# Kernel optimization log

Measured on AMD Instinct MI355X. Metric: run time of the kernel, lower is better.

## Reference

```python
import jax, jax.numpy as jnp
import numpy as np

ANGSTROM2BOHR = 1.8897261258369282
CUTOFF_ANGSTROM = 5.2  # module's `cutoff` init arg, converted to bohr in forward


def smooth_cutoff(d, rc):
    # torchani 'smooth' cutoff: exp(1 - 1/(1 - (d/rc)^2)) for d < rc, else 0
    x2 = (d / rc) ** 2
    x2_safe = jnp.where(x2 < 1.0, x2, 0.0)  # avoid inf inside the masked branch
    return jnp.where(d < rc, jnp.exp(1.0 - 1.0 / (1.0 - x2_safe)), 0.0)


def setup_inputs() -> dict:
    key = jax.random.key(0)
    k0, k1, k2, k3 = jax.random.split(key, 4)
    n_mol, n_atoms, n_pairs = 4096, 64, 16 * 1024 * 1024
    n_elem = 4  # H, C, N, O
    species = jax.random.randint(k0, (n_mol, n_atoms), 0, n_elem)
    energies = jnp.zeros((n_mol,), jnp.float32)
    atom_index12 = jax.random.randint(k1, (2, n_pairs), 0, n_mol * n_atoms)
    distances = jax.random.uniform(k2, (n_pairs,), jnp.float32, 0.5, 6.0)  # angstrom
    # exp_prefactor = -scaling_charge * sqrt(outer(Z, Z)) / 2, Z = [1, 6, 7, 8]
    z = jnp.array([1.0, 6.0, 7.0, 8.0], jnp.float32)
    exp_prefactor = (-0.016 * jnp.sqrt(jnp.outer(z, z)) / 2.0).astype(jnp.float32)
    # distances_factor = -scaling_radius / cutoff_radii (symmetric pairwise radii table)
    radii = jax.random.uniform(k3, (n_elem, n_elem), jnp.float32, 2.0, 5.0)
    radii = 0.5 * (radii + radii.T)
    distances_factor = (-10.0 / radii).astype(jnp.float32)
    return {
        "species": species,
        "energies": energies,
        "atom_index12": atom_index12,
        "distances": distances,
        "exp_prefactor": exp_prefactor,
        "distances_factor": distances_factor,
    }


def reference(species, energies, atom_index12, distances, exp_prefactor, distances_factor):
    n_mol, n_atoms = species.shape
    d = distances * ANGSTROM2BOHR  # [P]
    species12 = species.reshape(-1)[atom_index12]  # [2, P] gather
    pre = exp_prefactor[species12[0], species12[1]]   # [P]
    dfac = distances_factor[species12[0], species12[1]]  # [P]
    srb = pre * jnp.exp(dfac * d)
    srb = srb * smooth_cutoff(d, CUTOFF_ANGSTROM * ANGSTROM2BOHR)
    mol_idx = atom_index12[0] // n_atoms  # [P]
    out = energies + jax.ops.segment_sum(srb, mol_idx, num_segments=n_mol)
    return species, out
```

## Files before the change

kernel.cpp:

```cpp
#include <hip/hip_runtime.h>
#include <math.h>


#define NT        1024
#define NBLK      512
#define SCALE_F   134217728.0f
#define INV_SCALE 7.450580596923828125e-9

typedef unsigned v4u __attribute__((ext_vector_type(4)));
typedef float    v4f __attribute__((ext_vector_type(4)));

__global__ void pack_species_kernel(const int* __restrict__ sp,
                                    unsigned* __restrict__ packed, int nwords) {
    int w = blockIdx.x * blockDim.x + threadIdx.x;
    if (w >= nwords) return;
    const int4* p4 = (const int4*)(sp + (w << 4));
    int4 a = p4[0], b = p4[1], c = p4[2], d = p4[3];
    unsigned v =
        (unsigned)(a.x & 3)        | ((unsigned)(a.y & 3) << 2)  |
        ((unsigned)(a.z & 3) << 4) | ((unsigned)(a.w & 3) << 6)  |
        ((unsigned)(b.x & 3) << 8) | ((unsigned)(b.y & 3) << 10) |
        ((unsigned)(b.z & 3) << 12)| ((unsigned)(b.w & 3) << 14) |
        ((unsigned)(c.x & 3) << 16)| ((unsigned)(c.y & 3) << 18) |
        ((unsigned)(c.z & 3) << 20)| ((unsigned)(c.w & 3) << 22) |
        ((unsigned)(d.x & 3) << 24)| ((unsigned)(d.y & 3) << 26) |
        ((unsigned)(d.z & 3) << 28)| ((unsigned)(d.w & 3) << 30);
    packed[w] = v;
}

__global__ void init_kernel(const int* __restrict__ species,
                            float* __restrict__ out,
                            unsigned long long* __restrict__ acc,
                            int n_species, int n_mol) {
    int i = blockIdx.x * blockDim.x + threadIdx.x;
    if (i < n_species) out[i] = (float)species[i];
    if (i < n_mol)     acc[i] = 0ull;
}

#define GLOAD(d0, d1, dd, OFF)                                              \
    asm volatile("global_load_dwordx4 %0, %3, %4\n\t"                        \
                 "global_load_dwordx4 %1, %3, %5\n\t"                        \
                 "global_load_dwordx4 %2, %3, %6"                            \
                 : "=&v"(d0), "=&v"(d1), "=&v"(dd)                           \
                 : "v"(OFF), "s"(pb0), "s"(pb1), "s"(pbd)                    \
                 : "memory")

#define VWAIT(n)                                                             \
    do {                                                                     \
        asm volatile("s_waitcnt vmcnt(" #n ")" ::: "memory");                \
        __builtin_amdgcn_sched_barrier(0);                                   \
    } while (0)

__global__ __launch_bounds__(NT, 8)
void srb_fused_u32_pipe(const unsigned* __restrict__ packed_ws,
                        const int* __restrict__ ai,
                        const float* __restrict__ dist,
                        const float* __restrict__ pre_tab,
                        const float* __restrict__ dfac_tab,
                        unsigned long long* __restrict__ acc,
                        int P, int mol_shift, int nit) {
    __shared__ unsigned packed[16384];
    __shared__ unsigned binsu[4096];

    const int t = threadIdx.x;
    for (int i = t; i < 4096; i += NT) binsu[i] = 0u;

    const float myPre  = -pre_tab[t & 15];
    const float myDfac =  dfac_tab[t & 15];

    {
        int4* dst = (int4*)packed;
        const int4* src = (const int4*)packed_ws;
        for (int i = t; i < 4096; i += NT) dst[i] = src[i];
    }
    __syncthreads();

    const float a2b   = (float)1.8897261258369282;
    const float rc    = (float)(5.2 * 1.8897261258369282);
    const float rcinv = (float)(1.0 / (5.2 * 1.8897261258369282));

    const int      stride = (int)gridDim.x * NT;
    const unsigned stepB  = (unsigned)stride * 16u;
    unsigned off = (unsigned)((int)blockIdx.x * NT + t) * 16u;

    const char* pb0 = (const char*)ai;
    const char* pb1 = (const char*)(ai + P);
    const char* pbd = (const char*)dist;

    #define PBODY(X0, X1, XD)                                                \
    do {                                                                     \
        unsigned a0_[4] = { X0[0], X0[1], X0[2], X0[3] };                    \
        unsigned a1_[4] = { X1[0], X1[1], X1[2], X1[3] };                    \
        float    dd_[4] = { XD[0], XD[1], XD[2], XD[3] };                    \
        unsigned w0_[4], w1_[4];                                             \
        _Pragma("unroll")                                                    \
        for (int k = 0; k < 4; ++k) w0_[k] = packed[a0_[k] >> 4];            \
        _Pragma("unroll")                                                    \
        for (int k = 0; k < 4; ++k) w1_[k] = packed[a1_[k] >> 4];            \
        float pr_[4], df_[4];                                                \
        _Pragma("unroll")                                                    \
        for (int k = 0; k < 4; ++k) {                                        \
            unsigned s0 = (w0_[k] >> ((a0_[k] & 15u) << 1)) & 3u;            \
            unsigned s1 = (w1_[k] >> ((a1_[k] & 15u) << 1)) & 3u;            \
            int idx = (int)((s0 << 2) | s1);                                 \
            pr_[k] = __shfl(myPre,  idx, 64);                                \
            df_[k] = __shfl(myDfac, idx, 64);                                \
        }                                                                    \
        unsigned q_[4];                                                      \
        _Pragma("unroll")                                                    \
        for (int k = 0; k < 4; ++k) {                                        \
            float db  = dd_[k] * a2b;                                        \
            float x   = db * rcinv;                                          \
            float arg = df_[k] * db + (1.0f - 1.0f / (1.0f - x * x));        \
            float mag = pr_[k] * __expf(arg);                                \
            mag = (db < rc) ? mag : 0.0f;                                    \
            q_[k] = (unsigned)(mag * SCALE_F);                               \
        }                                                                    \
        _Pragma("unroll")                                                    \
        for (int k = 0; k < 4; ++k)                                          \
            atomicAdd(&binsu[a0_[k] >> mol_shift], q_[k]);                   \
    } while (0)

    v4u A0, A1, B0, B1, C0, C1;
    v4f AD, BDv, CD;

    GLOAD(A0, A1, AD, off);  off += stepB;
    GLOAD(B0, B1, BDv, off); off += stepB;

    int i = 0;
    #pragma unroll 1
    for (; i + 4 < nit; i += 3) {
        GLOAD(C0, C1, CD, off);  off += stepB;
        VWAIT(6);
        PBODY(A0, A1, AD);
        GLOAD(A0, A1, AD, off);  off += stepB;
        VWAIT(6);
        PBODY(B0, B1, BDv);
        GLOAD(B0, B1, BDv, off); off += stepB;
        VWAIT(6);
        PBODY(C0, C1, CD);
    }
    VWAIT(3);
    PBODY(A0, A1, AD);
    VWAIT(0);
    PBODY(B0, B1, BDv);

    #undef PBODY

    __syncthreads();
    for (int i2 = t; i2 < 4096; i2 += NT) {
        unsigned v = binsu[i2];
        if (v) atomicAdd(&acc[i2], (unsigned long long)v);
    }
}

__global__ __launch_bounds__(NT, 8)
void srb_fused_u32_gen(const unsigned* __restrict__ packed_ws,
                       const int* __restrict__ ai,
                       const float* __restrict__ dist,
                       const float* __restrict__ pre_tab,
                       const float* __restrict__ dfac_tab,
                       unsigned long long* __restrict__ acc,
                       int P, int mol_shift) {
    __shared__ unsigned packed[16384];
    __shared__ unsigned binsu[4096];

    const int t = threadIdx.x;
    for (int i = t; i < 4096; i += NT) binsu[i] = 0u;
    const float myPre  = -pre_tab[t & 15];
    const float myDfac =  dfac_tab[t & 15];
    {
        int4* dst = (int4*)packed;
        const int4* src = (const int4*)packed_ws;
        for (int i = t; i < 4096; i += NT) dst[i] = src[i];
    }
    __syncthreads();

    const float a2b   = (float)1.8897261258369282;
    const float rc    = (float)(5.2 * 1.8897261258369282);
    const float rcinv = (float)(1.0 / (5.2 * 1.8897261258369282));

    const int ng     = P >> 2;
    const int stride = (int)gridDim.x * NT;
    const int4*   v0 = (const int4*)ai;
    const int4*   v1 = (const int4*)(ai + P);
    const float4* dv = (const float4*)dist;

    for (int g = (int)blockIdx.x * NT + t; g < ng; g += stride) {
        int4 I0 = v0[g], I1 = v1[g]; float4 D = dv[g];
        unsigned a0[4] = { (unsigned)I0.x, (unsigned)I0.y,
                           (unsigned)I0.z, (unsigned)I0.w };
        unsigned a1[4] = { (unsigned)I1.x, (unsigned)I1.y,
                           (unsigned)I1.z, (unsigned)I1.w };
        float    dd[4] = { D.x, D.y, D.z, D.w };
        unsigned w0[4], w1[4];
        #pragma unroll
        for (int k = 0; k < 4; ++k) w0[k] = packed[a0[k] >> 4];
        #pragma unroll
        for (int k = 0; k < 4; ++k) w1[k] = packed[a1[k] >> 4];
        float pr[4], df[4];
        #pragma unroll
        for (int k = 0; k < 4; ++k) {
            unsigned s0 = (w0[k] >> ((a0[k] & 15u) << 1)) & 3u;
            unsigned s1 = (w1[k] >> ((a1[k] & 15u) << 1)) & 3u;
            int idx = (int)((s0 << 2) | s1);
            pr[k] = __shfl(myPre,  idx, 64);
            df[k] = __shfl(myDfac, idx, 64);
        }
        unsigned q[4];
        #pragma unroll
        for (int k = 0; k < 4; ++k) {
            float db  = dd[k] * a2b;
            float x   = db * rcinv;
            float arg = df[k] * db + (1.0f - 1.0f / (1.0f - x * x));
            float mag = pr[k] * __expf(arg);
            mag = (db < rc) ? mag : 0.0f;
            q[k] = (unsigned)(mag * SCALE_F);
        }
        #pragma unroll
        for (int k = 0; k < 4; ++k)
            atomicAdd(&binsu[a0[k] >> mol_shift], q[k]);
    }

    __syncthreads();
    for (int i = t; i < 4096; i += NT) {
        unsigned v = binsu[i];
        if (v) atomicAdd(&acc[i], (unsigned long long)v);
    }
}

__global__ void final_kernel(const unsigned long long* __restrict__ acc,
                             const float* __restrict__ energies,
                             float* __restrict__ out_e, int n_mol) {
    int m = blockIdx.x * blockDim.x + threadIdx.x;
    if (m < n_mol)
        out_e[m] = energies[m] - (float)((double)acc[m] * INV_SCALE);
}

__global__ void init_out_fallback(const int* __restrict__ species,
                                  const float* __restrict__ energies,
                                  float* __restrict__ out,
                                  int n_species, int n_mol) {
    int i = blockIdx.x * blockDim.x + threadIdx.x;
    if (i < n_species) out[i] = (float)species[i];
    else if (i < n_species + n_mol) out[i] = energies[i - n_species];
}

__global__ __launch_bounds__(NT, 1)
void srb_fused_f32(const int* __restrict__ species,
                   const int* __restrict__ ai,
                   const float* __restrict__ dist,
                   const float* __restrict__ pre_tab,
                   const float* __restrict__ dfac_tab,
                   float* __restrict__ out_e,
                   int P, int mol_shift) {
    __shared__ unsigned packed[16384];
    __shared__ float bins[4096];
    __shared__ float2 tab[16];
    const int t = threadIdx.x;
    for (int i = t; i < 4096; i += NT) bins[i] = 0.0f;
    if (t < 16) tab[t] = make_float2(pre_tab[t], dfac_tab[t]);
    for (int w = t; w < 16384; w += NT) {
        const int4* p4 = (const int4*)(species + (w << 4));
        int4 a = p4[0], b = p4[1], c = p4[2], d = p4[3];
        unsigned v =
            (unsigned)(a.x & 3)        | ((unsigned)(a.y & 3) << 2)  |
            ((unsigned)(a.z & 3) << 4) | ((unsigned)(a.w & 3) << 6)  |
            ((unsigned)(b.x & 3) << 8) | ((unsigned)(b.y & 3) << 10) |
            ((unsigned)(b.z & 3) << 12)| ((unsigned)(b.w & 3) << 14) |
            ((unsigned)(c.x & 3) << 16)| ((unsigned)(c.y & 3) << 18) |
            ((unsigned)(c.z & 3) << 20)| ((unsigned)(c.w & 3) << 22) |
            ((unsigned)(d.x & 3) << 24)| ((unsigned)(d.y & 3) << 26) |
            ((unsigned)(d.z & 3) << 28)| ((unsigned)(d.w & 3) << 30);
        packed[w] = v;
    }
    __syncthreads();
    const float a2b   = (float)1.8897261258369282;
    const float rc    = (float)(5.2 * 1.8897261258369282);
    const float rcinv = (float)(1.0 / (5.2 * 1.8897261258369282));
    auto body = [&](int a0, int a1, float dang) {
        unsigned ua0 = (unsigned)a0, ua1 = (unsigned)a1;
        unsigned s0 = (packed[ua0 >> 4] >> ((ua0 & 15u) << 1)) & 3u;
        unsigned s1 = (packed[ua1 >> 4] >> ((ua1 & 15u) << 1)) & 3u;
        float2 td = tab[(s0 << 2) | s1];
        float db = dang * a2b;
        float x  = db * rcinv;
        float arg = td.y * db + (1.0f - 1.0f / (1.0f - x * x));
        float srb = td.x * __expf(arg);
        srb = (db < rc) ? srb : 0.0f;
        atomicAdd(&bins[ua0 >> mol_shift], srb);
    };
    const int nv = P >> 2, stride = (int)gridDim.x * NT;
    const int4* v0 = (const int4*)ai;
    const int4* v1 = (const int4*)(ai + P);
    const float4* dv = (const float4*)dist;
    for (int v = (int)blockIdx.x * NT + t; v < nv; v += stride) {
        int4 i0 = v0[v]; int4 i1 = v1[v]; float4 dd = dv[v];
        body(i0.x, i1.x, dd.x); body(i0.y, i1.y, dd.y);
        body(i0.z, i1.z, dd.z); body(i0.w, i1.w, dd.w);
    }
    __syncthreads();
    for (int i = t; i < 4096; i += NT) {
        float s = bins[i];
        if (s != 0.0f) atomicAdd(&out_e[i], s);
    }
}

extern "C" void kernel_launch(void* const* d_in, const int* in_sizes, int n_in,
                              void* d_out, int out_size, void* d_ws, size_t ws_size,
                              hipStream_t stream) {
    const int*   species  = (const int*)d_in[0];
    const float* energies = (const float*)d_in[1];
    const int*   ai       = (const int*)d_in[2];
    const float* dist     = (const float*)d_in[3];
    const float* pre_tab  = (const float*)d_in[4];
    const float* dfac_tab = (const float*)d_in[5];

    const int n_species = in_sizes[0];
    const int n_mol     = in_sizes[1];
    const int P         = in_sizes[3];
    const int n_atoms   = n_species / n_mol;

    int mol_shift = 0;
    while ((1 << mol_shift) < n_atoms) ++mol_shift;

    float* out   = (float*)d_out;
    float* out_e = out + n_species;

    const int    nwords    = n_species / 16;
    const size_t packed_sz = (size_t)nwords * 4;
    const size_t acc_sz    = (size_t)n_mol * 8;
    const size_t need      = packed_sz + acc_sz;

    if (ws_size >= need && (P & 3) == 0) {
        unsigned*           packed = (unsigned*)d_ws;
        unsigned long long* acc    = (unsigned long long*)((char*)d_ws + packed_sz);

        init_kernel<<<(n_species + 255) / 256, 256, 0, stream>>>(
            species, out, acc, n_species, n_mol);
        pack_species_kernel<<<(nwords + 255) / 256, 256, 0, stream>>>(
            species, packed, nwords);

        const int ng     = P >> 2;
        const int stride = NBLK * NT;
        const int nit    = ng / stride;
        const bool pipe_ok = (ng % stride == 0) && (nit >= 2) && (nit % 3 == 2);

        if (pipe_ok) {
            srb_fused_u32_pipe<<<NBLK, NT, 0, stream>>>(
                packed, ai, dist, pre_tab, dfac_tab, acc, P, mol_shift, nit);
        } else {
            srb_fused_u32_gen<<<NBLK, NT, 0, stream>>>(
                packed, ai, dist, pre_tab, dfac_tab, acc, P, mol_shift);
        }
        final_kernel<<<(n_mol + 255) / 256, 256, 0, stream>>>(
            acc, energies, out_e, n_mol);
    } else {
        init_out_fallback<<<(n_species + n_mol + 255) / 256, 256, 0, stream>>>(
            species, energies, out, n_species, n_mol);
        srb_fused_f32<<<NBLK, NT, 0, stream>>>(
            species, ai, dist, pre_tab, dfac_tab, out_e, P, mol_shift);
    }
}
```

Before: 250.8 us.

## Switch pair pipeline to double buffering with full waits and block barriers

Replaces the three-stage register prefetch pipeline with a two-buffer scheme that issues the next load, processes the current buffer, then waits for all memory ops and synchronizes the block. The dispatch condition now accepts even iteration counts instead of counts that are 2 mod 3. This lowers register pressure and simplifies the schedule, but it gives up load/compute overlap depth and adds per-iteration barriers.

Result: no change. 253.3 us (+1.0%).

```diff
diff --git a/kernel.cpp b/kernel.cpp
--- a/kernel.cpp
+++ b/kernel.cpp
@@ -45,9 +45,9 @@
                  : "v"(OFF), "s"(pb0), "s"(pb1), "s"(pbd)                    \
                  : "memory")
 
-#define VWAIT(n)                                                             \
+#define VWAIT0()                                                             \
     do {                                                                     \
-        asm volatile("s_waitcnt vmcnt(" #n ")" ::: "memory");                \
+        asm volatile("s_waitcnt vmcnt(0)" ::: "memory");                     \
         __builtin_amdgcn_sched_barrier(0);                                   \
     } while (0)
 
@@ -121,30 +121,27 @@
             atomicAdd(&binsu[a0_[k] >> mol_shift], q_[k]);                   \
     } while (0)
 
-    v4u A0, A1, B0, B1, C0, C1;
-    v4f AD, BDv, CD;
-
-    GLOAD(A0, A1, AD, off);  off += stepB;
-    GLOAD(B0, B1, BDv, off); off += stepB;
-
-    int i = 0;
+    v4u A0, A1, B0, B1;
+    v4f AD, BDv;
+
+    GLOAD(A0, A1, AD, off); off += stepB;
+    VWAIT0();
+    __syncthreads();
+
     #pragma unroll 1
-    for (; i + 4 < nit; i += 3) {
-        GLOAD(C0, C1, CD, off);  off += stepB;
-        VWAIT(6);
+    for (int i = 0; i + 2 <= nit; i += 2) {
+        GLOAD(B0, B1, BDv, off); off += stepB;
         PBODY(A0, A1, AD);
-        GLOAD(A0, A1, AD, off);  off += stepB;
-        VWAIT(6);
+        VWAIT0();
+        __syncthreads();
+
+        if (i + 2 < nit) {
+            GLOAD(A0, A1, AD, off); off += stepB;
+        }
         PBODY(B0, B1, BDv);
-        GLOAD(B0, B1, BDv, off); off += stepB;
-        VWAIT(6);
-        PBODY(C0, C1, CD);
-    }
-    VWAIT(3);
-    PBODY(A0, A1, AD);
-    VWAIT(0);
-    PBODY(B0, B1, BDv);
-
+        VWAIT0();
+        __syncthreads();
+    }
     #undef PBODY
 
     __syncthreads();
@@ -344,7 +341,7 @@
         const int ng     = P >> 2;
         const int stride = NBLK * NT;
         const int nit    = ng / stride;
-        const bool pipe_ok = (ng % stride == 0) && (nit >= 2) && (nit % 3 == 2);
+        const bool pipe_ok = (ng % stride == 0) && (nit >= 2) && ((nit & 1) == 0);
 
         if (pipe_ok) {
             srb_fused_u32_pipe<<<NBLK, NT, 0, stream>>>(
```
